# Kernel optimization log

Hardware: AMD Instinct MI355X
Metric: run time of the kernel (lower is better)

The kernel has to match this reference:

```python
import jax, jax.numpy as jnp
import numpy as np

EPS1 = 1e-8
EPS2 = 1e-5
H_BW = 1.0  # bandwidth h
MSE_W = 1.0
CTX_W = 1.0
PERC_W = 0.02


def _contextual_similarity(out_feat, tgt_feat):
    """Batched contextual similarity (Mechrez et al. 2018).

    out_feat, tgt_feat: [B, C, Hf, Wf]. Returns scalar (mean over batch).
    Matches the torch loop-over-samples / loop-over-target-vectors math,
    fully vectorized as one batched pairwise-cosine + softmax + max.
    """
    B, C = out_feat.shape[0], out_feat.shape[1]
    # X, Y: [B, N, C] with N = Hf*Wf spatial positions
    X = out_feat.reshape(B, C, -1).transpose(0, 2, 1)
    Y = tgt_feat.reshape(B, C, -1).transpose(0, 2, 1)
    X = X - X.mean(axis=1, keepdims=True)  # center per channel over positions
    Y = Y - Y.mean(axis=1, keepdims=True)
    xn = jnp.linalg.norm(X, axis=2)  # [B, N]
    yn = jnp.linalg.norm(Y, axis=2)  # [B, N]
    # cosine distance d[b, x, y] = 1 - <X_x, Y_y> / (|X_x||Y_y| + eps1)
    S = jnp.einsum('bxc,byc->bxy', X, Y)
    d = 1.0 - S / (xn[:, :, None] * yn[:, None, :] + EPS1)
    # normalize by min over target vectors y (torch: dxy.min(dim=0) with dxy [Ny, Nx])
    d_ = d / (d.min(axis=2, keepdims=True) + EPS2)
    w = jnp.exp((1.0 - d_) / H_BW)
    c = w / w.sum(axis=2, keepdims=True)  # softmax over y per x
    # torch: cxy.max(dim=1)[0].mean() -> max over x for each y, mean over y
    CS = c.max(axis=1).mean(axis=1)  # [B]
    return CS.mean()


def _mse(a, b):
    return jnp.mean((a - b) ** 2)


def setup_inputs() -> dict:
    key = jax.random.key(0)
    k1, k2, k3, k4 = jax.random.split(key, 4)
    outputs = jax.random.normal(k1, (4, 3, 256, 256), dtype=jnp.float32)
    targets = jax.random.normal(k2, (4, 3, 256, 256), dtype=jnp.float32)
    output_features = jax.random.normal(k3, (4, 256, 64, 64), dtype=jnp.float32)
    target_features = jax.random.normal(k4, (4, 256, 64, 64), dtype=jnp.float32)
    return {"outputs": outputs, "targets": targets,
            "output_features": output_features, "target_features": target_features}


def reference(outputs, targets, output_features, target_features):
    loss = MSE_W * _mse(outputs, targets)
    loss = loss - CTX_W * jnp.log(_contextual_similarity(output_features, target_features))
    loss = loss + PERC_W * _mse(output_features, target_features)
    return loss
```

## Files before the change

### kernel.cpp

```cpp
#include <hip/hip_runtime.h>
#include <hip/hip_bf16.h>
#include <cstdint>

#define EPS2f 1e-5f

typedef __bf16 bf16x8 __attribute__((ext_vector_type(8)));
typedef float floatx4 __attribute__((ext_vector_type(4)));
typedef _Float16 half8 __attribute__((ext_vector_type(8)));
typedef __fp16 fp16x2 __attribute__((ext_vector_type(2)));

static constexpr int Bn = 4, Cn = 256, Nn = 4096;

static constexpr size_t MSE1P = 0;
static constexpr size_t MSE2P = 256;
static constexpr size_t CSP   = 1536;
static constexpr size_t MEANX = 2560;
static constexpr size_t MEANY = 3584;
static constexpr size_t IXN   = 4608;
static constexpr size_t IYN   = 20992;
static constexpr size_t DMIN  = 37376;
static constexpr size_t RSUM  = 53760;
static constexpr size_t XCO   = 70144;
static constexpr size_t YCO   = 70144 + 2097152;
static constexpr size_t SOFF  = 70144 + 2 * 2097152;

__device__ __forceinline__ unsigned short f2bf(float f) {
    unsigned u = __float_as_uint(f);
    u += 0x7fffu + ((u >> 16) & 1u);
    return (unsigned short)(u >> 16);
}

__global__ __launch_bounds__(256) void prep1(const float4* __restrict__ outs,
                                             const float4* __restrict__ tgts,
                                             const float4* __restrict__ of4,
                                             const float4* __restrict__ tf4,
                                             float* __restrict__ ws) {
    const int bid = blockIdx.x, t = threadIdx.x;
    __shared__ float red[12];
    if (bid < 1024) {
        const int c = bid & 255, b = bid >> 8;
        const float4* po = of4 + ((size_t)b * Cn + c) * (Nn / 4);
        const float4* pt = tf4 + ((size_t)b * Cn + c) * (Nn / 4);
        float so = 0.f, st = 0.f, sq = 0.f;
        for (int i = t; i < 1024; i += 256) {
            float4 o = po[i], q = pt[i];
            so += o.x + o.y + o.z + o.w;
            st += q.x + q.y + q.z + q.w;
            float dx = o.x - q.x, dy = o.y - q.y, dz = o.z - q.z, dw = o.w - q.w;
            sq += dx * dx + dy * dy + dz * dz + dw * dw;
        }
        for (int m = 1; m < 64; m <<= 1) {
            so += __shfl_xor(so, m); st += __shfl_xor(st, m); sq += __shfl_xor(sq, m);
        }
        if ((t & 63) == 0) { int w = t >> 6; red[w * 3] = so; red[w * 3 + 1] = st; red[w * 3 + 2] = sq; }
        __syncthreads();
        if (t == 0) {
            so = red[0] + red[3] + red[6] + red[9];
            st = red[1] + red[4] + red[7] + red[10];
            sq = red[2] + red[5] + red[8] + red[11];
            ws[MEANX + b * Cn + c] = so * (1.f / 4096.f);
            ws[MEANY + b * Cn + c] = st * (1.f / 4096.f);
            ws[MSE2P + bid] = sq;
        }
    } else if (bid < 1216) {
        const int base = bid - 1024;
        float sq = 0.f;
        for (int i = base * 256 + t; i < 196608; i += 192 * 256) {
            float4 a = outs[i], b4 = tgts[i];
            float dx = a.x - b4.x, dy = a.y - b4.y, dz = a.z - b4.z, dw = a.w - b4.w;
            sq += dx * dx + dy * dy + dz * dz + dw * dw;
        }
        for (int m = 1; m < 64; m <<= 1) sq += __shfl_xor(sq, m);
        if ((t & 63) == 0) red[t >> 6] = sq;
        __syncthreads();
        if (t == 0) ws[MSE1P + base] = red[0] + red[1] + red[2] + red[3];
    } else {
        const int i = (bid - 1216) * 256 + t;
        ws[DMIN + i] = (i < 16384) ? __builtin_inff() : 0.f;
    }
}

__global__ __launch_bounds__(256) void center_fused(const float* __restrict__ ofeat,
                                                    const float* __restrict__ tfeat,
                                                    float* __restrict__ ws) {
    const int b = blockIdx.y, nb = blockIdx.x, z = blockIdx.z;
    const float* feat = z ? tfeat : ofeat;
    const float* mean = ws + (z ? MEANY : MEANX);
    unsigned short* outb = (unsigned short*)(ws + (z ? YCO : XCO));
    float* inv = ws + (z ? IYN : IXN);
    __shared__ float mean_s[256];
    __shared__ float sq_s[256];
    const int t = threadIdx.x;
    mean_s[t] = mean[b * Cn + t];
    __syncthreads();
    const int pos = t & 63, cg = t >> 6;
    const int n = nb * 64 + pos;
    const float* fb = feat + (size_t)b * Cn * Nn;
    unsigned short* ob = outb + ((size_t)b * Nn + n) * Cn;
    float ss = 0.f;
    for (int c0 = cg * 64; c0 < cg * 64 + 64; c0 += 8) {
        unsigned short tmp[8];
        #pragma unroll
        for (int u = 0; u < 8; ++u) {
            float v = fb[(size_t)(c0 + u) * Nn + n] - mean_s[c0 + u];
            ss += v * v;
            tmp[u] = f2bf(v);
        }
        uint4 pk;
        pk.x = (unsigned)tmp[0] | ((unsigned)tmp[1] << 16);
        pk.y = (unsigned)tmp[2] | ((unsigned)tmp[3] << 16);
        pk.z = (unsigned)tmp[4] | ((unsigned)tmp[5] << 16);
        pk.w = (unsigned)tmp[6] | ((unsigned)tmp[7] << 16);
        *(uint4*)(ob + c0) = pk;
    }
    sq_s[t] = ss;
    __syncthreads();
    if (t < 64) {
        float s = sq_s[t] + sq_s[t + 64] + sq_s[t + 128] + sq_s[t + 192];
        inv[(size_t)b * Nn + nb * 64 + t] = 1.f / sqrtf(s);
    }
}

__global__ __launch_bounds__(256) void gemm_store(const unsigned short* __restrict__ Xc,
                                                  const unsigned short* __restrict__ Yc,
                                                  const float* __restrict__ ixn,
                                                  const float* __restrict__ iyn,
                                                  float* __restrict__ dmin,
                                                  _Float16* __restrict__ S) {
    __shared__ __align__(16) unsigned short smem[16384];
    __shared__ float ixn_s[128], iyn_s[128];

    const int t = threadIdx.x;
    const int bx = blockIdx.x, by = blockIdx.y, b = blockIdx.z;
    const size_t nb = (size_t)b * Nn;

    if (t < 128) ixn_s[t] = ixn[nb + bx * 128 + t];
    else iyn_s[t - 128] = iyn[nb + by * 128 + (t - 128)];

    const int wid = t >> 6, lane = t & 63;
    const int wm = wid >> 1, wn = wid & 1;
    const int lr = lane & 15, lq = lane >> 4;
    const int srow = t >> 2, sq = t & 3;

    const unsigned short* Ag = Xc + (nb + bx * 128) * Cn;
    const unsigned short* Bg = Yc + (nb + by * 128) * Cn;
    const unsigned short* Ga0 = Ag + (size_t)srow * Cn + sq * 8;
    const unsigned short* Ga1 = Ag + (size_t)(srow + 64) * Cn + sq * 8;
    const unsigned short* Gb0 = Bg + (size_t)srow * Cn + sq * 8;
    const unsigned short* Gb1 = Bg + (size_t)(srow + 64) * Cn + sq * 8;
    const int wA0 = (sq * 128 + srow) * 8;
    const int wA1 = (sq * 128 + srow + 64) * 8;

    floatx4 acc[4][4];
    #pragma unroll
    for (int i = 0; i < 4; i++)
        #pragma unroll
        for (int j = 0; j < 4; j++) acc[i][j] = (floatx4){0.f, 0.f, 0.f, 0.f};

    {
        uint4 a0 = *(const uint4*)Ga0, a1 = *(const uint4*)Ga1;
        uint4 b0 = *(const uint4*)Gb0, b1 = *(const uint4*)Gb1;
        *(uint4*)(smem + wA0) = a0;
        *(uint4*)(smem + wA1) = a1;
        *(uint4*)(smem + 4096 + wA0) = b0;
        *(uint4*)(smem + 4096 + wA1) = b1;
    }
    __syncthreads();

    #pragma unroll
    for (int ks = 0; ks < 8; ks++) {
        const int cur = (ks & 1) * 8192, nxt = 8192 - cur;
        uint4 a0, a1, b0, b1;
        if (ks < 7) {
            a0 = *(const uint4*)(Ga0 + (ks + 1) * 32);
            a1 = *(const uint4*)(Ga1 + (ks + 1) * 32);
            b0 = *(const uint4*)(Gb0 + (ks + 1) * 32);
            b1 = *(const uint4*)(Gb1 + (ks + 1) * 32);
        }
        bf16x8 af[4], bv[4];
        #pragma unroll
        for (int i = 0; i < 4; i++)
            af[i] = *(const bf16x8*)(smem + cur + (lq * 128 + wm * 64 + i * 16 + lr) * 8);
        #pragma unroll
        for (int j = 0; j < 4; j++)
            bv[j] = *(const bf16x8*)(smem + cur + 4096 + (lq * 128 + wn * 64 + j * 16 + lr) * 8);
        #pragma unroll
        for (int i = 0; i < 4; i++)
            #pragma unroll
            for (int j = 0; j < 4; j++)
                acc[i][j] = __builtin_amdgcn_mfma_f32_16x16x32_bf16(af[i], bv[j], acc[i][j], 0, 0, 0);
        if (ks < 7) {
            *(uint4*)(smem + nxt + wA0) = a0;
            *(uint4*)(smem + nxt + wA1) = a1;
            *(uint4*)(smem + nxt + 4096 + wA0) = b0;
            *(uint4*)(smem + nxt + 4096 + wA1) = b1;
            __syncthreads();
        }
    }

    float ix[16];
    #pragma unroll
    for (int i = 0; i < 4; i++)
        #pragma unroll
        for (int r = 0; r < 4; r++) ix[i * 4 + r] = ixn_s[wm * 64 + i * 16 + lq * 4 + r];
    float rmin[16];
    #pragma unroll
    for (int k = 0; k < 16; k++) rmin[k] = __builtin_inff();
    #pragma unroll
    for (int i = 0; i < 4; i++)
        #pragma unroll
        for (int j = 0; j < 4; j++) {
            const float iy = iyn_s[wn * 64 + j * 16 + lr];
            #pragma unroll
            for (int r = 0; r < 4; r++)
                rmin[i * 4 + r] = fminf(rmin[i * 4 + r], 1.f - acc[i][j][r] * ix[i * 4 + r] * iy);
        }
    #pragma unroll
    for (int m = 1; m < 16; m <<= 1)
        #pragma unroll
        for (int k = 0; k < 16; k++) rmin[k] = fminf(rmin[k], __shfl_xor(rmin[k], m));
    if (lr == 0) {
        #pragma unroll
        for (int i = 0; i < 4; i++)
            #pragma unroll
            for (int r = 0; r < 4; r++)
                atomicMin((int*)&dmin[nb + bx * 128 + wm * 64 + i * 16 + lq * 4 + r],
                          __float_as_int(rmin[i * 4 + r]));
    }
    __syncthreads();

    #pragma unroll
    for (int i = 0; i < 4; i++) {
        const int xlocal = wm * 64 + i * 16 + lq * 4;
        #pragma unroll
        for (int j = 0; j < 4; j++) {
            const int ylocal = wn * 64 + j * 16 + lr;
            const float iy = iyn_s[ylocal];
            float c0 = acc[i][j][0] * ix[i * 4 + 0] * iy;
            float c1 = acc[i][j][1] * ix[i * 4 + 1] * iy;
            float c2 = acc[i][j][2] * ix[i * 4 + 2] * iy;
            float c3 = acc[i][j][3] * ix[i * 4 + 3] * iy;
            fp16x2 p0 = __builtin_amdgcn_cvt_pkrtz(c0, c1);
            fp16x2 p1 = __builtin_amdgcn_cvt_pkrtz(c2, c3);
            *(float2*)(smem + ylocal * 128 + (xlocal ^ ((ylocal & 15) * 8))) =
                make_float2(__builtin_bit_cast(float, p0), __builtin_bit_cast(float, p1));
        }
    }
    __syncthreads();

    #pragma unroll
    for (int p = 0; p < 8; p++) {
        const int yl = wid * 32 + p * 4 + (lane >> 4);
        const int ch = lane & 15;
        uint4 v = *(const uint4*)(smem + yl * 128 + ((ch * 8) ^ ((yl & 15) * 8)));
        *(uint4*)(S + (nb + by * 128 + yl) * (size_t)Nn + bx * 128 + ch * 8) = v;
    }
}

__global__ __launch_bounds__(256) void b1_rsum(const _Float16* __restrict__ S,
                                               const float* __restrict__ dmin,
                                               float* __restrict__ rsum) {
    __shared__ float red[32 * 65];
    const int t = threadIdx.x;
    const int x0 = blockIdx.x * 64, ys = blockIdx.y, b = blockIdx.z;
    const int chunk = t & 7, yg = t >> 3;
    const int xbase = x0 + chunk * 8;
    const size_t gb = (size_t)b * Nn;

    float invd[8], av[8];
    #pragma unroll
    for (int u = 0; u < 8; u++) {
        float dm = dmin[gb + xbase + u];
        invd[u] = 1.f / (dm + EPS2f);
        av[u] = 1.f - invd[u];
    }
    float s[8];
    #pragma unroll
    for (int u = 0; u < 8; u++) s[u] = 0.f;

    for (int k = 0; k < 16; k++) {
        const int y = ys * 512 + yg + 32 * k;
        half8 hv = *(const half8*)(S + (gb + y) * Nn + xbase);
        #pragma unroll
        for (int u = 0; u < 8; u++)
            s[u] += __expf(fmaf((float)hv[u], invd[u], av[u]));
    }
    #pragma unroll
    for (int u = 0; u < 8; u++) red[yg * 65 + chunk * 8 + u] = s[u];
    __syncthreads();
    if (t < 64) {
        float rs = 0.f;
        #pragma unroll 8
        for (int g = 0; g < 32; g++) rs += red[g * 65 + t];
        atomicAdd(&rsum[gb + x0 + t], rs);
    }
}

__global__ __launch_bounds__(256) void b2_cmax(const _Float16* __restrict__ S,
                                               const float* __restrict__ dmin,
                                               const float* __restrict__ rsum,
                                               float* __restrict__ csp) {
    __shared__ float ps[512 * 20];
    __shared__ float red2[16];
    const int t = threadIdx.x, b = blockIdx.y;
    const size_t gb = (size_t)b * Nn;
    for (int i = t; i < Nn; i += 256) {
        float iv = 1.f / (dmin[gb + i] + EPS2f);
        float gg = 1.f - iv - __logf(rsum[gb + i]);
        int c = i >> 3, e = i & 7;
        ps[c * 20 + e * 2] = iv;
        ps[c * 20 + e * 2 + 1] = gg;
    }
    __syncthreads();

    const int lanegrp = t & 15, yloc = t >> 4;
    const int y = blockIdx.x * 16 + yloc;
    const _Float16* Sy = S + (gb + y) * Nn;

    float cm = 0.f;
    for (int k = 0; k < 32; k++) {
        const int chunk = lanegrp + 16 * k;
        half8 hv = *(const half8*)(Sy + chunk * 8);
        const float* pp = &ps[chunk * 20];
        float4 p01 = *(const float4*)(pp);
        float4 p23 = *(const float4*)(pp + 4);
        float4 p45 = *(const float4*)(pp + 8);
        float4 p67 = *(const float4*)(pp + 12);
        float iv[8] = {p01.x, p01.z, p23.x, p23.z, p45.x, p45.z, p67.x, p67.z};
        float gg[8] = {p01.y, p01.w, p23.y, p23.w, p45.y, p45.w, p67.y, p67.w};
        #pragma unroll
        for (int u = 0; u < 8; u++)
            cm = fmaxf(cm, __expf(fmaf((float)hv[u], iv[u], gg[u])));
    }
    #pragma unroll
    for (int m = 1; m < 16; m <<= 1) cm = fmaxf(cm, __shfl_xor(cm, m));
    if (lanegrp == 0) red2[yloc] = cm;
    __syncthreads();
    if (t == 0) {
        float s2 = 0.f;
        #pragma unroll
        for (int i = 0; i < 16; i++) s2 += red2[i];
        csp[b * 256 + blockIdx.x] = s2;
    }
}

__global__ __launch_bounds__(256) void finalize_kernel(const float* __restrict__ ws,
                                                       float* __restrict__ out) {
    const int t = threadIdx.x;
    float s1 = 0.f, s2 = 0.f, s3 = 0.f;
    if (t < 192) s1 = ws[MSE1P + t];
    for (int i = t; i < 1024; i += 256) { s2 += ws[MSE2P + i]; s3 += ws[CSP + i]; }
    for (int m = 1; m < 64; m <<= 1) {
        s1 += __shfl_xor(s1, m); s2 += __shfl_xor(s2, m); s3 += __shfl_xor(s3, m);
    }
    __shared__ float red[12];
    if ((t & 63) == 0) { int w = t >> 6; red[w * 3] = s1; red[w * 3 + 1] = s2; red[w * 3 + 2] = s3; }
    __syncthreads();
    if (t == 0) {
        s1 = red[0] + red[3] + red[6] + red[9];
        s2 = red[1] + red[4] + red[7] + red[10];
        s3 = red[2] + red[5] + red[8] + red[11];
        float cs = s3 * (1.f / 16384.f);
        out[0] = s1 * (1.f / 786432.f) - logf(cs) + 0.02f * s2 * (1.f / 4194304.f);
    }
}

extern "C" void kernel_launch(void* const* d_in, const int* in_sizes, int n_in,
                              void* d_out, int out_size, void* d_ws, size_t ws_size,
                              hipStream_t stream) {
    const float* outputs = (const float*)d_in[0];
    const float* targets = (const float*)d_in[1];
    const float* ofeat   = (const float*)d_in[2];
    const float* tfeat   = (const float*)d_in[3];
    float* ws  = (float*)d_ws;
    float* out = (float*)d_out;

    unsigned short* Xc = (unsigned short*)(ws + XCO);
    unsigned short* Yc = (unsigned short*)(ws + YCO);
    _Float16* S = (_Float16*)(ws + SOFF);

    prep1<<<1344, 256, 0, stream>>>((const float4*)outputs, (const float4*)targets,
                                    (const float4*)ofeat, (const float4*)tfeat, ws);
    center_fused<<<dim3(Nn / 64, Bn, 2), 256, 0, stream>>>(ofeat, tfeat, ws);
    gemm_store<<<dim3(Nn / 128, Nn / 128, Bn), 256, 0, stream>>>(Xc, Yc, ws + IXN, ws + IYN,
                                                                 ws + DMIN, S);
    b1_rsum<<<dim3(64, 8, Bn), 256, 0, stream>>>(S, ws + DMIN, ws + RSUM);
    b2_cmax<<<dim3(Nn / 16, Bn), 256, 0, stream>>>(S, ws + DMIN, ws + RSUM, ws + CSP);
    finalize_kernel<<<1, 256, 0, stream>>>(ws, out);
}
```

Before: 237.9 us.

## Store cosine similarity matrix in fp8 with XCD-aware block remap and exp2

```diff
diff --git a/kernel.cpp b/kernel.cpp
--- a/kernel.cpp
+++ b/kernel.cpp
@@ -3,11 +3,11 @@
 #include <cstdint>
 
 #define EPS2f 1e-5f
+#define LOG2E 1.44269504f
 
 typedef __bf16 bf16x8 __attribute__((ext_vector_type(8)));
 typedef float floatx4 __attribute__((ext_vector_type(4)));
-typedef _Float16 half8 __attribute__((ext_vector_type(8)));
-typedef __fp16 fp16x2 __attribute__((ext_vector_type(2)));
+typedef float floatx2 __attribute__((ext_vector_type(2)));
 
 static constexpr int Bn = 4, Cn = 256, Nn = 4096;
 
@@ -126,12 +126,16 @@
                                                   const float* __restrict__ ixn,
                                                   const float* __restrict__ iyn,
                                                   float* __restrict__ dmin,
-                                                  _Float16* __restrict__ S) {
+                                                  unsigned char* __restrict__ S) {
     __shared__ __align__(16) unsigned short smem[16384];
     __shared__ float ixn_s[128], iyn_s[128];
 
     const int t = threadIdx.x;
-    const int bx = blockIdx.x, by = blockIdx.y, b = blockIdx.z;
+    const int lin = blockIdx.x;
+    const int xcd = lin & 7, idx = lin >> 3;
+    const int b = xcd >> 1;
+    const int by = (xcd & 1) * 16 + (idx & 15);
+    const int bx = idx >> 4;
     const size_t nb = (size_t)b * Nn;
 
     if (t < 128) ixn_s[t] = ixn[nb + bx * 128 + t];
@@ -227,8 +231,8 @@
                 atomicMin((int*)&dmin[nb + bx * 128 + wm * 64 + i * 16 + lq * 4 + r],
                           __float_as_int(rmin[i * 4 + r]));
     }
-    __syncthreads();
-
+
+    unsigned char* Tb = (unsigned char*)smem;
     #pragma unroll
     for (int i = 0; i < 4; i++) {
         const int xlocal = wm * 64 + i * 16 + lq * 4;
@@ -240,24 +244,23 @@
             float c1 = acc[i][j][1] * ix[i * 4 + 1] * iy;
             float c2 = acc[i][j][2] * ix[i * 4 + 2] * iy;
             float c3 = acc[i][j][3] * ix[i * 4 + 3] * iy;
-            fp16x2 p0 = __builtin_amdgcn_cvt_pkrtz(c0, c1);
-            fp16x2 p1 = __builtin_amdgcn_cvt_pkrtz(c2, c3);
-            *(float2*)(smem + ylocal * 128 + (xlocal ^ ((ylocal & 15) * 8))) =
-                make_float2(__builtin_bit_cast(float, p0), __builtin_bit_cast(float, p1));
-        }
-    }
-    __syncthreads();
-
-    #pragma unroll
-    for (int p = 0; p < 8; p++) {
-        const int yl = wid * 32 + p * 4 + (lane >> 4);
-        const int ch = lane & 15;
-        uint4 v = *(const uint4*)(smem + yl * 128 + ((ch * 8) ^ ((yl & 15) * 8)));
-        *(uint4*)(S + (nb + by * 128 + yl) * (size_t)Nn + bx * 128 + ch * 8) = v;
-    }
-}
-
-__global__ __launch_bounds__(256) void b1_rsum(const _Float16* __restrict__ S,
+            int pk = __builtin_amdgcn_cvt_pk_fp8_f32(c0, c1, 0, false);
+            pk = __builtin_amdgcn_cvt_pk_fp8_f32(c2, c3, pk, true);
+            *(int*)(Tb + ylocal * 128 + (xlocal ^ ((ylocal & 7) << 4))) = pk;
+        }
+    }
+    __syncthreads();
+
+    #pragma unroll
+    for (int p = 0; p < 4; p++) {
+        const int row = p * 32 + wid * 8 + (lane >> 3);
+        const int ch = lane & 7;
+        uint4 v = *(const uint4*)(Tb + row * 128 + ((ch * 16) ^ ((row & 7) << 4)));
+        *(uint4*)(S + (nb + by * 128 + row) * (size_t)Nn + bx * 128 + ch * 16) = v;
+    }
+}
+
+__global__ __launch_bounds__(256) void b1_rsum(const unsigned char* __restrict__ S,
                                                const float* __restrict__ dmin,
                                                float* __restrict__ rsum) {
     __shared__ float red[32 * 65];
@@ -267,12 +270,12 @@
     const int xbase = x0 + chunk * 8;
     const size_t gb = (size_t)b * Nn;
 
-    float invd[8], av[8];
+    float ivl[8], avl[8];
     #pragma unroll
     for (int u = 0; u < 8; u++) {
-        float dm = dmin[gb + xbase + u];
-        invd[u] = 1.f / (dm + EPS2f);
-        av[u] = 1.f - invd[u];
+        float iv = 1.f / (dmin[gb + xbase + u] + EPS2f);
+        ivl[u] = iv * LOG2E;
+        avl[u] = (1.f - iv) * LOG2E;
     }
     float s[8];
     #pragma unroll
@@ -280,10 +283,15 @@
 
     for (int k = 0; k < 16; k++) {
         const int y = ys * 512 + yg + 32 * k;
-        half8 hv = *(const half8*)(S + (gb + y) * Nn + xbase);
+        uint2 w = *(const uint2*)(S + (gb + y) * Nn + xbase);
+        floatx2 v0 = __builtin_amdgcn_cvt_pk_f32_fp8(w.x, false);
+        floatx2 v1 = __builtin_amdgcn_cvt_pk_f32_fp8(w.x, true);
+        floatx2 v2 = __builtin_amdgcn_cvt_pk_f32_fp8(w.y, false);
+        floatx2 v3 = __builtin_amdgcn_cvt_pk_f32_fp8(w.y, true);
+        float c[8] = {v0[0], v0[1], v1[0], v1[1], v2[0], v2[1], v3[0], v3[1]};
         #pragma unroll
         for (int u = 0; u < 8; u++)
-            s[u] += __expf(fmaf((float)hv[u], invd[u], av[u]));
+            s[u] += exp2f(fmaf(c[u], ivl[u], avl[u]));
     }
     #pragma unroll
     for (int u = 0; u < 8; u++) red[yg * 65 + chunk * 8 + u] = s[u];
@@ -296,7 +304,7 @@
     }
 }
 
-__global__ __launch_bounds__(256) void b2_cmax(const _Float16* __restrict__ S,
+__global__ __launch_bounds__(256) void b2_cmax(const unsigned char* __restrict__ S,
                                                const float* __restrict__ dmin,
                                                const float* __restrict__ rsum,
                                                float* __restrict__ csp) {
@@ -306,21 +314,27 @@
     const size_t gb = (size_t)b * Nn;
     for (int i = t; i < Nn; i += 256) {
         float iv = 1.f / (dmin[gb + i] + EPS2f);
-        float gg = 1.f - iv - __logf(rsum[gb + i]);
+        float ivl = iv * LOG2E;
+        float ggl = (1.f - iv) * LOG2E - __log2f(rsum[gb + i]);
         int c = i >> 3, e = i & 7;
-        ps[c * 20 + e * 2] = iv;
-        ps[c * 20 + e * 2 + 1] = gg;
+        ps[c * 20 + e * 2] = ivl;
+        ps[c * 20 + e * 2 + 1] = ggl;
     }
     __syncthreads();
 
     const int lanegrp = t & 15, yloc = t >> 4;
     const int y = blockIdx.x * 16 + yloc;
-    const _Float16* Sy = S + (gb + y) * Nn;
-
-    float cm = 0.f;
+    const unsigned char* Sy = S + (gb + y) * Nn;
+
+    float cm = -1e30f;
     for (int k = 0; k < 32; k++) {
         const int chunk = lanegrp + 16 * k;
-        half8 hv = *(const half8*)(Sy + chunk * 8);
+        uint2 w = *(const uint2*)(Sy + chunk * 8);
+        floatx2 v0 = __builtin_amdgcn_cvt_pk_f32_fp8(w.x, false);
+        floatx2 v1 = __builtin_amdgcn_cvt_pk_f32_fp8(w.x, true);
+        floatx2 v2 = __builtin_amdgcn_cvt_pk_f32_fp8(w.y, false);
+        floatx2 v3 = __builtin_amdgcn_cvt_pk_f32_fp8(w.y, true);
+        float c[8] = {v0[0], v0[1], v1[0], v1[1], v2[0], v2[1], v3[0], v3[1]};
         const float* pp = &ps[chunk * 20];
         float4 p01 = *(const float4*)(pp);
         float4 p23 = *(const float4*)(pp + 4);
@@ -330,11 +344,11 @@
         float gg[8] = {p01.y, p01.w, p23.y, p23.w, p45.y, p45.w, p67.y, p67.w};
         #pragma unroll
         for (int u = 0; u < 8; u++)
-            cm = fmaxf(cm, __expf(fmaf((float)hv[u], iv[u], gg[u])));
+            cm = fmaxf(cm, fmaf(c[u], iv[u], gg[u]));
     }
     #pragma unroll
     for (int m = 1; m < 16; m <<= 1) cm = fmaxf(cm, __shfl_xor(cm, m));
-    if (lanegrp == 0) red2[yloc] = cm;
+    if (lanegrp == 0) red2[yloc] = exp2f(cm);
     __syncthreads();
     if (t == 0) {
         float s2 = 0.f;
@@ -377,13 +391,12 @@
 
     unsigned short* Xc = (unsigned short*)(ws + XCO);
     unsigned short* Yc = (unsigned short*)(ws + YCO);
-    _Float16* S = (_Float16*)(ws + SOFF);
+    unsigned char* S = (unsigned char*)(ws + SOFF);
 
     prep1<<<1344, 256, 0, stream>>>((const float4*)outputs, (const float4*)targets,
                                     (const float4*)ofeat, (const float4*)tfeat, ws);
     center_fused<<<dim3(Nn / 64, Bn, 2), 256, 0, stream>>>(ofeat, tfeat, ws);
-    gemm_store<<<dim3(Nn / 128, Nn / 128, Bn), 256, 0, stream>>>(Xc, Yc, ws + IXN, ws + IYN,
-                                                                 ws + DMIN, S);
+    gemm_store<<<4096, 256, 0, stream>>>(Xc, Yc, ws + IXN, ws + IYN, ws + DMIN, S);
     b1_rsum<<<dim3(64, 8, Bn), 256, 0, stream>>>(S, ws + DMIN, ws + RSUM);
     b2_cmax<<<dim3(Nn / 16, Bn), 256, 0, stream>>>(S, ws + DMIN, ws + RSUM, ws + CSP);
     finalize_kernel<<<1, 256, 0, stream>>>(ws, out);
```

Measured after the change: 257.8 us. 1.08x slower.
